# Optimization experiments

Measured on AMD Instinct MI355X. Metric: run time of the kernel, lower is better.

Reference implementation:

```python
import jax, jax.numpy as jnp
import numpy as np

NUM_HEADS = 16


def _rope(x, c, s):
    # x: [T, H, D]; c, s: [T, D/2] -> rotate-half RoPE over full head_dim
    d2 = c.shape[-1]
    x1, x2 = x[..., :d2], x[..., d2:]
    c = c[:, None, :]
    s = s[:, None, :]
    return jnp.concatenate([x1 * c - x2 * s, x2 * c + x1 * s], axis=-1)


def setup_inputs() -> dict:
    key = jax.random.key(0)
    ks = jax.random.split(key, 4)
    B, L, dim = 8, 1024, 1024
    T = B * L
    D = dim // NUM_HEADS
    hidden_states = jax.random.normal(ks[0], (T, dim), dtype=jnp.float32)
    w_qkv = jax.random.normal(ks[1], (dim, 3 * dim), dtype=jnp.float32) * (dim ** -0.5)
    b_qkv = jnp.zeros((3 * dim,), dtype=jnp.float32)
    w_proj = jax.random.normal(ks[2], (dim, dim), dtype=jnp.float32) * (dim ** -0.5)
    b_proj = jnp.zeros((dim,), dtype=jnp.float32)
    # RoPE tables: positions restart at 0 for each packed sequence
    pos = jnp.tile(jnp.arange(L, dtype=jnp.float32), B)  # [T]
    inv_freq = 1.0 / (10000.0 ** (jnp.arange(0, D, 2, dtype=jnp.float32) / D))  # [D/2]
    freqs = pos[:, None] * inv_freq[None, :]  # [T, D/2]
    emb = jnp.concatenate([freqs, freqs], axis=-1)  # [T, D]
    cos = jnp.cos(emb)
    sin = jnp.sin(emb)
    cu_seqlens = (jnp.arange(B + 1, dtype=jnp.int32) * L)
    return {"hidden_states": hidden_states, "cos": cos, "sin": sin,
            "w_qkv": w_qkv, "b_qkv": b_qkv, "w_proj": w_proj, "b_proj": b_proj,
            "cu_seqlens": cu_seqlens}


def reference(hidden_states, cos, sin, w_qkv, b_qkv, w_proj, b_proj, cu_seqlens):
    T, dim = hidden_states.shape
    H = NUM_HEADS
    D = dim // H
    B = cu_seqlens.shape[0] - 1  # equal-length packed sequences
    L = T // B

    qkv = hidden_states @ w_qkv + b_qkv            # [T, 3*dim]
    qkv = qkv.reshape(T, 3, H, D)
    q, k, v = qkv[:, 0], qkv[:, 1], qkv[:, 2]       # [T, H, D]

    # module chunks cos/sin in half along last dim before apply_rotary_emb
    c = cos[..., : D // 2].astype(jnp.float32)
    s = sin[..., : D // 2].astype(jnp.float32)
    q = _rope(q.astype(jnp.float32), c, s).astype(hidden_states.dtype)
    k = _rope(k.astype(jnp.float32), c, s).astype(hidden_states.dtype)

    # varlen flash attention == block-diagonal attention; equal lengths -> reshape
    qb = q.reshape(B, L, H, D)
    kb = k.reshape(B, L, H, D)
    vb = v.reshape(B, L, H, D)
    scale = D ** -0.5
    scores = jnp.einsum("bqhd,bkhd->bhqk", qb, kb) * scale  # [B, H, L, L]
    probs = jax.nn.softmax(scores, axis=-1)
    out = jnp.einsum("bhqk,bkhd->bqhd", probs, vb)           # [B, L, H, D]
    out = out.reshape(T, dim)
    return out @ w_proj + b_proj
```

## Files before the change

### kernel.cpp

```cpp
#include <hip/hip_runtime.h>

typedef unsigned short ushort_t;
typedef __attribute__((ext_vector_type(8))) short short8;
typedef __attribute__((ext_vector_type(4))) float f32x4;

#define AS1 __attribute__((address_space(1)))
#define AS3 __attribute__((address_space(3)))

__device__ __forceinline__ ushort_t f2bf(float f) {
  unsigned int u = __builtin_bit_cast(unsigned int, f);
  u += 0x7fffu + ((u >> 16) & 1u);
  return (ushort_t)(u >> 16);
}

__device__ __forceinline__ unsigned int pack_bf2(float a, float b) {
  unsigned int ua = __builtin_bit_cast(unsigned int, a) + 0x8000u;
  unsigned int ub = __builtin_bit_cast(unsigned int, b) + 0x8000u;
  return (ua >> 16) | (ub & 0xffff0000u);
}

#if defined(__has_builtin)
#if __has_builtin(__builtin_amdgcn_cvt_pk_bf16_f32)
#define HAVE_CVT_PK_BF16 1
#endif
#if __has_builtin(__builtin_amdgcn_exp2f)
#define HAVE_EXP2 1
#endif
#endif

__device__ __forceinline__ unsigned int pack2(float a, float b) {
#ifdef HAVE_CVT_PK_BF16
  typedef __attribute__((ext_vector_type(2))) __bf16 bf2_t;
  bf2_t r = __builtin_amdgcn_cvt_pk_bf16_f32(a, b);
  return __builtin_bit_cast(unsigned int, r);
#else
  return pack_bf2(a, b);
#endif
}

__device__ __forceinline__ float fast_exp2(float x) {
#ifdef HAVE_EXP2
  return __builtin_amdgcn_exp2f(x);
#else
  return exp2f(x);
#endif
}

__device__ __forceinline__ void load_lds16(const ushort_t* g, ushort_t* l) {
  __builtin_amdgcn_global_load_lds((AS1 void*)g, (AS3 void*)l, 16, 0, 0);
}

#define MFMA16(a, b, c) __builtin_amdgcn_mfma_f32_16x16x32_bf16((a), (b), (c), 0, 0, 0)

__global__ __launch_bounds__(256) void k_prep(const float* __restrict__ hs,
                                              ushort_t* __restrict__ hsb,
                                              const float* __restrict__ wqkv,
                                              ushort_t* __restrict__ wqkvT,
                                              const float* __restrict__ wproj,
                                              ushort_t* __restrict__ wprojT) {
  __shared__ ushort_t t[64 * 65];
  const int bid = blockIdx.x;
  if (bid < 4096) {
    int i = bid * 256 + threadIdx.x;
    const float4* s4 = (const float4*)hs;
    float4 a = s4[(size_t)i * 2], b = s4[(size_t)i * 2 + 1];
    short8 o;
    o[0] = (short)f2bf(a.x); o[1] = (short)f2bf(a.y);
    o[2] = (short)f2bf(a.z); o[3] = (short)f2bf(a.w);
    o[4] = (short)f2bf(b.x); o[5] = (short)f2bf(b.y);
    o[6] = (short)f2bf(b.z); o[7] = (short)f2bf(b.w);
    *(short8*)(hsb + (size_t)i * 8) = o;
    return;
  }
  const float* src;
  ushort_t* dst;
  int C, bx, by;
  if (bid < 4864) { int idx = bid - 4096; src = wqkv; dst = wqkvT; C = 3072;
                    bx = idx % 48; by = idx / 48; }
  else            { int idx = bid - 4864; src = wproj; dst = wprojT; C = 1024;
                    bx = idx & 15; by = idx >> 4; }
  const int R = 1024;
  const int x0 = bx * 64, y0 = by * 64;
  const int c = threadIdx.x & 63, r0 = threadIdx.x >> 6;
#pragma unroll
  for (int i = 0; i < 16; ++i) {
    int r = r0 + i * 4;
    t[c * 65 + r] = f2bf(src[(size_t)(y0 + r) * C + x0 + c]);
  }
  __syncthreads();
#pragma unroll
  for (int i = 0; i < 16; ++i) {
    int rr = r0 + i * 4;
    dst[(size_t)(x0 + rr) * R + y0 + c] = t[rr * 65 + c];
  }
}

__global__ __launch_bounds__(512) void k_qkv_gemm_rope(
    const ushort_t* __restrict__ A, const ushort_t* __restrict__ Bt,
    const float* __restrict__ bias, const float* __restrict__ cosb,
    const float* __restrict__ sinb, ushort_t* __restrict__ Qb,
    ushort_t* __restrict__ Kb, ushort_t* __restrict__ Vp) {
  constexpr int K = 1024;
  __shared__ __align__(16) ushort_t As[256 * 64];
  __shared__ __align__(16) ushort_t Bs[128 * 64];
  const int tid = threadIdx.x, lane = tid & 63, wave = tid >> 6;
  const int quad = lane >> 4, ml = lane & 15;
  const int wm = wave & 3, wn = wave >> 2;
  const int L = blockIdx.x, xcd = L & 7, j = L >> 3;
  const int by = xcd * 4 + j / 24, bx = j % 24;
  const int m0 = by * 256, n0 = bx * 128;
  f32x4 acc[4][4] = {};

  for (int kt = 0; kt < K / 64; ++kt) {
    __syncthreads();
    {
      const int kk0 = kt * 64;
#pragma unroll
      for (int i = 0; i < 4; ++i) {
        int cch = i * 512 + tid;
        int r = cch >> 3, s = cch & 7, gs = s ^ (r & 7);
        load_lds16(A + (size_t)(m0 + r) * K + kk0 + gs * 8, As + cch * 8);
      }
#pragma unroll
      for (int i = 0; i < 2; ++i) {
        int cch = i * 512 + tid;
        int r = cch >> 3, s = cch & 7, gs = s ^ (r & 7);
        load_lds16(Bt + (size_t)(n0 + r) * K + kk0 + gs * 8, Bs + cch * 8);
      }
    }
    __syncthreads();
#pragma unroll
    for (int ks = 0; ks < 2; ++ks) {
      short8 af[4], bfr[4];
#pragma unroll
      for (int mb = 0; mb < 4; ++mb) {
        int row = wm * 64 + mb * 16 + ml;
        int gs = (ks * 4 + quad) ^ (row & 7);
        af[mb] = *(const short8*)(As + row * 64 + gs * 8);
      }
#pragma unroll
      for (int nb = 0; nb < 4; ++nb) {
        int row = wn * 64 + nb * 16 + ml;
        int gs = (ks * 4 + quad) ^ (row & 7);
        bfr[nb] = *(const short8*)(Bs + row * 64 + gs * 8);
      }
#pragma unroll
      for (int mb = 0; mb < 4; ++mb)
#pragma unroll
        for (int nb = 0; nb < 4; ++nb)
          acc[mb][nb] = MFMA16(af[mb], bfr[nb], acc[mb][nb]);
    }
  }

  const int ncol0 = n0 + wn * 64;
  const int sec = ncol0 >> 10;
  const int h = (ncol0 & 1023) >> 6;
  if (sec < 2) {
    ushort_t* dst = (sec == 0) ? Qb : Kb;
    const float qs = (sec == 0) ? 0.18033688011112042f : 1.0f;
#pragma unroll
    for (int mb = 0; mb < 4; ++mb) {
#pragma unroll
      for (int rg = 0; rg < 4; ++rg) {
        const int m = m0 + wm * 64 + mb * 16 + quad * 4 + rg;
        const int b = m >> 10, l = m & 1023;
        const size_t ob = ((size_t)(b * 16 + h) * 1024 + l) * 64;
#pragma unroll
        for (int nb = 0; nb < 2; ++nb) {
          const int d = nb * 16 + ml;
          float x1 = acc[mb][nb][rg] + bias[ncol0 + d];
          float x2 = acc[mb][nb + 2][rg] + bias[ncol0 + d + 32];
          float cv = cosb[(size_t)m * 64 + d] * qs;
          float sv = sinb[(size_t)m * 64 + d] * qs;
          dst[ob + d] = f2bf(x1 * cv - x2 * sv);
          dst[ob + d + 32] = f2bf(x2 * cv + x1 * sv);
        }
      }
    }
  } else {
    const int mrow = m0 + wm * 64;
    const int b = mrow >> 10, lB = mrow & 1023;
    ushort_t* vb = Vp + ((size_t)(b * 16 + h)) * 65536 + lB;
#pragma unroll
    for (int rg = 0; rg < 4; ++rg) {
#pragma unroll
      for (int nb = 0; nb < 4; ++nb) {
        const int d = nb * 16 + ml;
        const float bs = bias[ncol0 + d];
        uint2 w;
        w.x = pack_bf2(acc[0][nb][rg] + bs, acc[1][nb][rg] + bs);
        w.y = pack_bf2(acc[2][nb][rg] + bs, acc[3][nb][rg] + bs);
        *(uint2*)(vb + (size_t)d * 1024 + 16 * quad + 4 * rg) = w;
      }
    }
  }
}

__global__ __launch_bounds__(512, 4) void k_attn(const ushort_t* __restrict__ Qb,
                                                 const ushort_t* __restrict__ Kb,
                                                 const ushort_t* __restrict__ Vp,
                                                 ushort_t* __restrict__ Ob) {
  __shared__ __align__(16) ushort_t S[32768];
  const int tid = threadIdx.x, lane = tid & 63, wave = tid >> 6;
  const int quad = lane >> 4, ml = lane & 15;
  const int bh = blockIdx.x & 127, qt = blockIdx.x >> 7;
  const int q0 = qt * 256;
  const size_t base = (size_t)bh * 65536;

#pragma unroll
  for (int i = 0; i < 4; ++i) {
    int cch = i * 512 + tid;
    int r = cch >> 3, s = cch & 7, gs = s ^ (r & 7);
    load_lds16(Qb + base + (size_t)(q0 + r) * 64 + gs * 8, S + cch * 8);
  }

  const ushort_t* kg;
  const ushort_t* vg;
  ushort_t *kl, *vl;
  {
    int r = tid >> 3, gs = (tid & 7) ^ (r & 7);
    kg = Kb + base + (size_t)r * 64 + gs * 8;
    kl = S + 16384 + tid * 8;
    vg = Vp + base + (size_t)r * 1024 + gs * 8;
    vl = S + 24576 + tid * 8;
  }
  load_lds16(kg, kl); kg += 4096;
  load_lds16(vg, vl); vg += 64;
  __syncthreads();

  const int gsA = quad ^ (ml & 7);
  const int gsB = (4 + quad) ^ (ml & 7);
  const int h0 = (ml >> 1) ^ (quad * 4);

  short8 qf[2][2];
#pragma unroll
  for (int mb = 0; mb < 2; ++mb) {
    int rowoff = wave * 2048 + mb * 1024 + ml * 64;
    qf[mb][0] = *(const short8*)(S + rowoff + gsA * 8);
    qf[mb][1] = *(const short8*)(S + rowoff + gsB * 8);
  }
  __syncthreads();

  const ushort_t* kA = S + 16384 + ml * 64 + gsA * 8;
  const ushort_t* kB = S + 16384 + ml * 64 + gsB * 8;
  const ushort_t* pA = S + wave * 2048 + ml * 64 + gsA * 8;
  const ushort_t* pB = S + wave * 2048 + ml * 64 + gsB * 8;
  ushort_t* pwl = S + wave * 2048 + quad * 256 + (ml & 1) * 4;

  f32x4 Oacc[2][4] = {};
  float lsum[2][4] = {};

#define ATTN_STEP(CUR, LAST)                                                  \
  {                                                                           \
    if (!(LAST)) {                                                            \
      load_lds16(kg, kl + ((CUR) ^ 1) * 4096); kg += 4096;                    \
      load_lds16(vg, vl + ((CUR) ^ 1) * 4096); vg += 64;                      \
    }                                                                         \
    f32x4 Sacc[2][4] = {};                                                    \
    __builtin_amdgcn_s_setprio(1);                                            \
    _Pragma("unroll") for (int nb = 0; nb < 4; ++nb) {                        \
      short8 kfa = *(const short8*)(kA + (CUR) * 4096 + nb * 1024);           \
      short8 kfb = *(const short8*)(kB + (CUR) * 4096 + nb * 1024);           \
      Sacc[0][nb] = MFMA16(qf[0][0], kfa, Sacc[0][nb]);                       \
      Sacc[1][nb] = MFMA16(qf[1][0], kfa, Sacc[1][nb]);                       \
      Sacc[0][nb] = MFMA16(qf[0][1], kfb, Sacc[0][nb]);                       \
      Sacc[1][nb] = MFMA16(qf[1][1], kfb, Sacc[1][nb]);                       \
    }                                                                         \
    __builtin_amdgcn_s_setprio(0);                                            \
    _Pragma("unroll") for (int mb = 0; mb < 2; ++mb) {                        \
      _Pragma("unroll") for (int rg = 0; rg < 4; ++rg) {                      \
        float p0 = fast_exp2(Sacc[mb][0][rg]);                                \
        float p1 = fast_exp2(Sacc[mb][1][rg]);                                \
        float p2 = fast_exp2(Sacc[mb][2][rg]);                                \
        float p3 = fast_exp2(Sacc[mb][3][rg]);                                \
        lsum[mb][rg] += (p0 + p1) + (p2 + p3);                                \
        uint2 w;                                                              \
        w.x = pack2(p0, p1);                                                  \
        w.y = pack2(p2, p3);                                                  \
        int g8 = ((h0 ^ rg) & 7) * 8;                                         \
        *(uint2*)(pwl + mb * 1024 + rg * 64 + g8) = w;                        \
      }                                                                       \
    }                                                                         \
    __builtin_amdgcn_s_setprio(1);                                            \
    _Pragma("unroll") for (int ks = 0; ks < 2; ++ks) {                        \
      const ushort_t* pk = ks ? pB : pA;                                      \
      const ushort_t* vk = (ks ? kB : kA) + 8192 + (CUR) * 4096;              \
      short8 pf0 = *(const short8*)(pk);                                      \
      short8 pf1 = *(const short8*)(pk + 1024);                               \
      _Pragma("unroll") for (int nb = 0; nb < 4; ++nb) {                      \
        short8 vf = *(const short8*)(vk + nb * 1024);                         \
        Oacc[0][nb] = MFMA16(pf0, vf, Oacc[0][nb]);                           \
        Oacc[1][nb] = MFMA16(pf1, vf, Oacc[1][nb]);                           \
      }                                                                       \
    }                                                                         \
    __builtin_amdgcn_s_setprio(0);                                            \
    __syncthreads();                                                          \
  }

#pragma unroll 1
  for (int kt2 = 0; kt2 < 8; ++kt2) {
    ATTN_STEP(0, false)
    ATTN_STEP(1, kt2 == 7)
  }
#undef ATTN_STEP

  const int b = bh >> 4, h = bh & 15;
#pragma unroll
  for (int mb = 0; mb < 2; ++mb) {
#pragma unroll
    for (int rg = 0; rg < 4; ++rg) {
      float l = lsum[mb][rg];
      l += __shfl_xor(l, 1);
      l += __shfl_xor(l, 2);
      l += __shfl_xor(l, 4);
      l += __shfl_xor(l, 8);
      float inv = 1.f / l;
      int q = q0 + wave * 32 + mb * 16 + quad * 4 + rg;
      size_t ob = ((size_t)(b * 1024 + q)) * 1024 + h * 64;
#pragma unroll
      for (int nb = 0; nb < 4; ++nb)
        Ob[ob + nb * 16 + ml] = f2bf(Oacc[mb][nb][rg] * inv);
    }
  }
}

__global__ __launch_bounds__(256) void k_proj_gemm(const ushort_t* __restrict__ A,
                                                   const ushort_t* __restrict__ Bt,
                                                   const float* __restrict__ bias,
                                                   float* __restrict__ out) {
  constexpr int K = 1024;
  __shared__ __align__(16) ushort_t As[128 * 128];
  __shared__ __align__(16) ushort_t Bs[128 * 128];
  const int tid = threadIdx.x, lane = tid & 63, wave = tid >> 6;
  const int quad = lane >> 4, ml = lane & 15;
  const int wm = wave & 1, wn = wave >> 1;
  const int L = blockIdx.x, xcd = L & 7, j = L >> 3;
  const int by = xcd * 8 + (j >> 3), bx = j & 7;
  const int m0 = by * 128, n0 = bx * 128;
  f32x4 acc[4][4] = {};

  for (int kt = 0; kt < K / 128; ++kt) {
    __syncthreads();
    {
      const int kk0 = kt * 128;
#pragma unroll
      for (int i = 0; i < 8; ++i) {
        int cch = i * 256 + tid;
        int r = cch >> 4, s = cch & 15, gs = s ^ (r & 15);
        load_lds16(A + (size_t)(m0 + r) * K + kk0 + gs * 8, As + cch * 8);
        load_lds16(Bt + (size_t)(n0 + r) * K + kk0 + gs * 8, Bs + cch * 8);
      }
    }
    __syncthreads();
#pragma unroll
    for (int ks = 0; ks < 4; ++ks) {
      short8 af[4], bfr[4];
#pragma unroll
      for (int mb = 0; mb < 4; ++mb) {
        int row = wm * 64 + mb * 16 + ml;
        int gs = (ks * 4 + quad) ^ (row & 15);
        af[mb] = *(const short8*)(As + row * 128 + gs * 8);
      }
#pragma unroll
      for (int nb = 0; nb < 4; ++nb) {
        int row = wn * 64 + nb * 16 + ml;
        int gs = (ks * 4 + quad) ^ (row & 15);
        bfr[nb] = *(const short8*)(Bs + row * 128 + gs * 8);
      }
#pragma unroll
      for (int mb = 0; mb < 4; ++mb)
#pragma unroll
        for (int nb = 0; nb < 4; ++nb)
          acc[mb][nb] = MFMA16(af[mb], bfr[nb], acc[mb][nb]);
    }
  }
#pragma unroll
  for (int mb = 0; mb < 4; ++mb) {
#pragma unroll
    for (int rg = 0; rg < 4; ++rg) {
      const int m = m0 + wm * 64 + mb * 16 + quad * 4 + rg;
#pragma unroll
      for (int nb = 0; nb < 4; ++nb) {
        const int n = n0 + wn * 64 + nb * 16 + ml;
        out[(size_t)m * 1024 + n] = acc[mb][nb][rg] + bias[n];
      }
    }
  }
}

extern "C" void kernel_launch(void* const* d_in, const int* in_sizes, int n_in,
                              void* d_out, int out_size, void* d_ws, size_t ws_size,
                              hipStream_t stream) {
  const float* hs = (const float*)d_in[0];
  const float* cosb = (const float*)d_in[1];
  const float* sinb = (const float*)d_in[2];
  const float* wqkv = (const float*)d_in[3];
  const float* bqkv = (const float*)d_in[4];
  const float* wproj = (const float*)d_in[5];
  const float* bproj = (const float*)d_in[6];
  float* out = (float*)d_out;

  char* ws = (char*)d_ws;
  ushort_t* hsb = (ushort_t*)(ws);
  ushort_t* wqkvT = (ushort_t*)(ws + (16u << 20));
  ushort_t* wprojT = (ushort_t*)(ws + (22u << 20));
  ushort_t* Qb = (ushort_t*)(ws + (24u << 20));
  ushort_t* Kb = (ushort_t*)(ws + (40u << 20));
  ushort_t* Vp = (ushort_t*)(ws + (56u << 20));
  ushort_t* attnb = hsb;

  k_prep<<<5120, 256, 0, stream>>>(hs, hsb, wqkv, wqkvT, wproj, wprojT);
  k_qkv_gemm_rope<<<768, 512, 0, stream>>>(hsb, wqkvT, bqkv, cosb, sinb,
                                           Qb, Kb, Vp);
  k_attn<<<512, 512, 0, stream>>>(Qb, Kb, Vp, attnb);
  k_proj_gemm<<<512, 256, 0, stream>>>(attnb, wprojT, bproj, out);
}
```

Measured before the change: 243.5 us.

## Pipeline QKV GEMM with 4-stage LDS ring and explicit waitcnt barriers

Restructures the QKV projection GEMM main loop from a single-buffered 64-wide K tile with two full syncthreads per step into a 4-deep ring of 32-wide K half-tiles. Async global-to-LDS loads are issued three stages ahead and tracked with manual vmcnt waits and raw s_barrier. MFMA bursts run at raised wave priority. The goal is to hide global load latency behind compute and cut barrier stalls, in exchange for more LDS, a new swizzle scheme and fragile hand-managed synchronisation.

New measurement: 256.6 us. +5.4%, slower.

```diff
diff --git a/kernel.cpp b/kernel.cpp
--- a/kernel.cpp
+++ b/kernel.cpp
@@ -51,6 +51,10 @@
 }
 
 #define MFMA16(a, b, c) __builtin_amdgcn_mfma_f32_16x16x32_bf16((a), (b), (c), 0, 0, 0)
+#define BAR() __builtin_amdgcn_s_barrier()
+#define SCHEDB() __builtin_amdgcn_sched_barrier(0)
+#define WAITV_(N) asm volatile("s_waitcnt vmcnt(" #N ")" ::: "memory")
+#define WAITV(N) WAITV_(N)
 
 __global__ __launch_bounds__(256) void k_prep(const float* __restrict__ hs,
                                               ushort_t* __restrict__ hsb,
@@ -101,8 +105,8 @@
     const float* __restrict__ sinb, ushort_t* __restrict__ Qb,
     ushort_t* __restrict__ Kb, ushort_t* __restrict__ Vp) {
   constexpr int K = 1024;
-  __shared__ __align__(16) ushort_t As[256 * 64];
-  __shared__ __align__(16) ushort_t Bs[128 * 64];
+  __shared__ __align__(16) ushort_t As[4][8192];
+  __shared__ __align__(16) ushort_t Bs[4][4096];
   const int tid = threadIdx.x, lane = tid & 63, wave = tid >> 6;
   const int quad = lane >> 4, ml = lane & 15;
   const int wm = wave & 3, wn = wave >> 2;
@@ -111,46 +115,78 @@
   const int m0 = by * 256, n0 = bx * 128;
   f32x4 acc[4][4] = {};
 
-  for (int kt = 0; kt < K / 64; ++kt) {
-    __syncthreads();
-    {
-      const int kk0 = kt * 64;
-#pragma unroll
-      for (int i = 0; i < 4; ++i) {
-        int cch = i * 512 + tid;
-        int r = cch >> 3, s = cch & 7, gs = s ^ (r & 7);
-        load_lds16(A + (size_t)(m0 + r) * K + kk0 + gs * 8, As + cch * 8);
-      }
-#pragma unroll
-      for (int i = 0; i < 2; ++i) {
-        int cch = i * 512 + tid;
-        int r = cch >> 3, s = cch & 7, gs = s ^ (r & 7);
-        load_lds16(Bt + (size_t)(n0 + r) * K + kk0 + gs * 8, Bs + cch * 8);
-      }
-    }
-    __syncthreads();
-#pragma unroll
-    for (int ks = 0; ks < 2; ++ks) {
-      short8 af[4], bfr[4];
-#pragma unroll
-      for (int mb = 0; mb < 4; ++mb) {
-        int row = wm * 64 + mb * 16 + ml;
-        int gs = (ks * 4 + quad) ^ (row & 7);
-        af[mb] = *(const short8*)(As + row * 64 + gs * 8);
-      }
-#pragma unroll
-      for (int nb = 0; nb < 4; ++nb) {
-        int row = wn * 64 + nb * 16 + ml;
-        int gs = (ks * 4 + quad) ^ (row & 7);
-        bfr[nb] = *(const short8*)(Bs + row * 64 + gs * 8);
-      }
-#pragma unroll
-      for (int mb = 0; mb < 4; ++mb)
-#pragma unroll
-        for (int nb = 0; nb < 4; ++nb)
-          acc[mb][nb] = MFMA16(af[mb], bfr[nb], acc[mb][nb]);
-    }
-  }
+  const ushort_t* ag[2];
+  ushort_t* al[2];
+  const ushort_t* bg;
+  ushort_t* bl;
+#pragma unroll
+  for (int i = 0; i < 2; ++i) {
+    int cch = i * 512 + tid;
+    int r = cch >> 2, s = cch & 3, gs = s ^ ((r >> 1) & 3);
+    ag[i] = A + (size_t)(m0 + r) * K + gs * 8;
+    al[i] = &As[0][0] + cch * 8;
+  }
+  {
+    int r = tid >> 2, s = tid & 3, gs = s ^ ((r >> 1) & 3);
+    bg = Bt + (size_t)(n0 + r) * K + gs * 8;
+    bl = &Bs[0][0] + tid * 8;
+  }
+
+  int afo[4], bfo[4];
+#pragma unroll
+  for (int mb = 0; mb < 4; ++mb) {
+    int row = wm * 64 + mb * 16 + ml;
+    afo[mb] = row * 32 + ((quad ^ ((row >> 1) & 3)) & 3) * 8;
+  }
+#pragma unroll
+  for (int nb = 0; nb < 4; ++nb) {
+    int row = wn * 64 + nb * 16 + ml;
+    bfo[nb] = row * 32 + ((quad ^ ((row >> 1) & 3)) & 3) * 8;
+  }
+
+#pragma unroll
+  for (int h = 0; h < 3; ++h) {
+    load_lds16(ag[0], al[0] + h * 8192); ag[0] += 32;
+    load_lds16(ag[1], al[1] + h * 8192); ag[1] += 32;
+    load_lds16(bg, bl + h * 4096); bg += 32;
+  }
+  WAITV(6);
+  BAR(); SCHEDB();
+
+#define HSTEP(BUF, NBUF, ISS, WN)                                             \
+  {                                                                           \
+    if (ISS) {                                                                \
+      load_lds16(ag[0], al[0] + (NBUF) * 8192); ag[0] += 32;                  \
+      load_lds16(ag[1], al[1] + (NBUF) * 8192); ag[1] += 32;                  \
+      load_lds16(bg, bl + (NBUF) * 4096); bg += 32;                           \
+    }                                                                         \
+    short8 af[4], bfr[4];                                                     \
+    _Pragma("unroll") for (int mb = 0; mb < 4; ++mb)                          \
+        af[mb] = *(const short8*)(&As[0][0] + (BUF) * 8192 + afo[mb]);        \
+    _Pragma("unroll") for (int nb = 0; nb < 4; ++nb)                          \
+        bfr[nb] = *(const short8*)(&Bs[0][0] + (BUF) * 4096 + bfo[nb]);       \
+    BAR(); SCHEDB();                                                          \
+    __builtin_amdgcn_s_setprio(1);                                            \
+    _Pragma("unroll") for (int mb = 0; mb < 4; ++mb)                          \
+      _Pragma("unroll") for (int nb = 0; nb < 4; ++nb)                        \
+          acc[mb][nb] = MFMA16(af[mb], bfr[nb], acc[mb][nb]);                 \
+    __builtin_amdgcn_s_setprio(0);                                            \
+    WAITV(WN);                                                                \
+    BAR(); SCHEDB();                                                          \
+  }
+
+#pragma unroll 1
+  for (int t = 0; t < 7; ++t) {
+    HSTEP(0, 3, 1, 6)
+    HSTEP(1, 0, 1, 6)
+    HSTEP(2, 1, 1, 6)
+    HSTEP(3, 2, 1, 6)
+  }
+  HSTEP(0, 3, 1, 6)
+  HSTEP(1, 0, 0, 3)
+  HSTEP(2, 0, 0, 0)
+  HSTEP(3, 0, 0, 0)
+#undef HSTEP
 
   const int ncol0 = n0 + wn * 64;
   const int sec = ncol0 >> 10;
```
